# Kernel tuning notes

Hardware: AMD Instinct MI355X
Metric: run time of the kernel (lower is better)

Reference implementation:

```python
import jax, jax.numpy as jnp
import numpy as np
import math

N_HEADS = 16
D_MODEL = 1024
M = D_MODEL // N_HEADS  # per-head dim = 64

def _kaiming_uniform(key, shape):
    # torch kaiming_uniform_ with a=sqrt(5) on [h, fan_in, fan_out]-style 3D tensor:
    # fan_in = shape[1] (size of dim 1), gain = sqrt(2/(1+a^2)) = sqrt(1/3)
    fan_in = shape[1]
    gain = math.sqrt(2.0 / (1.0 + 5.0))
    bound = gain * math.sqrt(3.0 / fan_in)
    return jax.random.uniform(key, shape, dtype=jnp.float32, minval=-bound, maxval=bound)

def setup_inputs() -> dict:
    key = jax.random.key(0)
    kx, kq, kk, kv, ko = jax.random.split(key, 5)
    x = jax.random.normal(kx, (4, 2048, D_MODEL), dtype=jnp.float32)
    W_q = _kaiming_uniform(kq, (N_HEADS, D_MODEL, M))
    W_k = _kaiming_uniform(kk, (N_HEADS, D_MODEL, M))
    W_v = _kaiming_uniform(kv, (N_HEADS, D_MODEL, M))
    W_o = _kaiming_uniform(ko, (N_HEADS, M, D_MODEL))
    return {"x": x, "W_q": W_q, "W_k": W_k, "W_v": W_v, "W_o": W_o}

def reference(x, W_q, W_k, W_v, W_o):
    # x: [b, s, d]; W_q/W_k/W_v: [h, d, m]; W_o: [h, m, d]
    q = jnp.einsum('bsd,hdm->bhsm', x, W_q)
    k = jnp.einsum('bsd,hdm->bhsm', x, W_k)
    v = jnp.einsum('bsd,hdm->bhsm', x, W_v)
    scale = 1.0 / math.sqrt(q.shape[-1])
    scores = jnp.einsum('bhsm,bhtm->bhst', q, k) * scale  # [b,h,s,s]
    attn = jax.nn.softmax(scores, axis=-1)
    ctx = jnp.einsum('bhst,bhtm->bhsm', attn, v)
    out = jnp.einsum('bhsm,hmd->bsd', ctx, W_o)  # sum over heads
    return out
```

## Files before the change

kernel.cpp:

```cpp
#include <hip/hip_runtime.h>
#include <hip/hip_bf16.h>

typedef __attribute__((ext_vector_type(8))) short short8;
typedef __attribute__((ext_vector_type(8))) _Float16 half8;
typedef __attribute__((ext_vector_type(4))) float f32x4;
typedef __attribute__((ext_vector_type(16))) float f32x16;
typedef __attribute__((ext_vector_type(4))) unsigned int uint4v;

#define NB 4
#define NH 16
#define NS 2048
#define ND 1024
#define NM 64
#define R_TOT 8192
#define N_QKV 3072
#define QKV_ONE 8388608
#define SCALE_Q 0.18033688011112042f

static __device__ __forceinline__ unsigned short f2h(float f) {
    _Float16 h = (_Float16)f;
    return __builtin_bit_cast(unsigned short, h);
}
static __device__ __forceinline__ unsigned cvtpk_h(float lo, float hiv) {
    unsigned r;
    asm("v_cvt_pkrtz_f16_f32 %0, %1, %2" : "=v"(r) : "v"(lo), "v"(hiv));
    return r;
}
static __device__ __forceinline__ void gl_lds16(const unsigned short* g, unsigned short* l) {
    __builtin_amdgcn_global_load_lds((const __attribute__((address_space(1))) void*)g,
                                     (__attribute__((address_space(3))) void*)l, 16, 0, 0);
}
static __device__ __forceinline__ half8 rd_swz(const unsigned short* base, int row, int col) {
    int byte = (row << 7) + (col << 1);
    byte ^= (row & 7) << 4;
    return *(const half8*)((const char*)base + byte);
}

__global__ __launch_bounds__(256) void k_convert_x(const float* __restrict__ x,
                                                   unsigned short* __restrict__ xh) {
    int i = blockIdx.x * 256 + threadIdx.x;
    const float4* xp = (const float4*)x;
    float4 v = xp[i];
    ushort4 o;
    o.x = f2h(v.x); o.y = f2h(v.y); o.z = f2h(v.z); o.w = f2h(v.w);
    ((ushort4*)xh)[i] = o;
}

__global__ __launch_bounds__(256) void k_convert_wqkv(const float* __restrict__ Wq,
                                                      const float* __restrict__ Wk,
                                                      const float* __restrict__ Wv,
                                                      unsigned short* __restrict__ BT) {
    int i = blockIdx.x * 256 + threadIdx.x;
    int d = i & 1023;
    int n = i >> 10;
    int w = n >> 10;
    int h = (n >> 6) & 15;
    int m = n & 63;
    const float* W = (w == 0) ? Wq : ((w == 1) ? Wk : Wv);
    float v = W[((size_t)h * ND + d) * NM + m];
    if (w == 0) v *= SCALE_Q;
    BT[i] = f2h(v);
}

__global__ __launch_bounds__(256) void k_convert_wo(const float* __restrict__ Wo,
                                                    unsigned short* __restrict__ BTo) {
    int i = blockIdx.x * 256 + threadIdx.x;
    int n = i & 1023;
    int d = i >> 10;
    BTo[i] = f2h(Wo[(size_t)n * ND + d]);
}

__global__ __launch_bounds__(256) void k_gemm_qkv(const unsigned short* __restrict__ A,
                                                  const unsigned short* __restrict__ BT,
                                                  unsigned short* __restrict__ qkv) {
    __shared__ unsigned short As[128 * 64];
    __shared__ unsigned short Bs[128 * 64];
    int tid = threadIdx.x;
    int bx = blockIdx.x;
    int rt = bx & 63;
    int ct = bx >> 6;
    int r0 = rt * 128, c0 = ct * 128;
    int lane = tid & 63, wid = tid >> 6;
    int l15 = lane & 15, grp = lane >> 4;
    int wr = (wid >> 1) * 64, wc = (wid & 1) * 64;

    f32x4 acc[4][4] = {};

    for (int k0 = 0; k0 < 1024; k0 += 64) {
        #pragma unroll
        for (int i = 0; i < 4; ++i) {
            int seg = wid * 4 + i;
            int row = seg * 8 + (lane >> 3);
            int sch = (lane & 7) ^ (row & 7);
            gl_lds16(A + (size_t)(r0 + row) * 1024 + k0 + sch * 8, As + seg * 512 + lane * 8);
            gl_lds16(BT + (size_t)(c0 + row) * 1024 + k0 + sch * 8, Bs + seg * 512 + lane * 8);
        }
        __syncthreads();
        #pragma unroll
        for (int ks = 0; ks < 64; ks += 32) {
            half8 af[4], bf[4];
            #pragma unroll
            for (int i = 0; i < 4; ++i)
                af[i] = rd_swz(As, wr + i * 16 + l15, ks + grp * 8);
            #pragma unroll
            for (int j = 0; j < 4; ++j)
                bf[j] = rd_swz(Bs, wc + j * 16 + l15, ks + grp * 8);
            #pragma unroll
            for (int i = 0; i < 4; ++i)
                #pragma unroll
                for (int j = 0; j < 4; ++j)
                    acc[i][j] = __builtin_amdgcn_mfma_f32_16x16x32_f16(af[i], bf[j], acc[i][j], 0, 0, 0);
        }
        __syncthreads();
    }
    #pragma unroll
    for (int j = 0; j < 4; ++j) {
        int n_base = c0 + wc + j * 16;
        int w = n_base >> 10;
        int nh = n_base + l15;
        int h = (nh >> 6) & 15;
        int m = nh & 63;
        if (w == 2) {
            unsigned short* outp = qkv + 2 * (size_t)QKV_ONE;
            #pragma unroll
            for (int i = 0; i < 4; ++i) {
                int rb = r0 + wr + i * 16 + grp * 4;
                int bb = rb >> 11, s = rb & 2047;
                ushort4 pv;
                pv.x = f2h(acc[i][j][0]);
                pv.y = f2h(acc[i][j][1]);
                pv.z = f2h(acc[i][j][2]);
                pv.w = f2h(acc[i][j][3]);
                *(ushort4*)(outp + ((size_t)(bb * NH + h) * NM + m) * NS + s) = pv;
            }
        } else {
            unsigned short* outp = qkv + (size_t)w * QKV_ONE;
            #pragma unroll
            for (int i = 0; i < 4; ++i) {
                int rb = r0 + wr + i * 16 + grp * 4;
                #pragma unroll
                for (int reg = 0; reg < 4; ++reg) {
                    int r = rb + reg;
                    int bb = r >> 11, s = r & 2047;
                    outp[((size_t)(bb * NH + h) * NS + s) * NM + m] = f2h(acc[i][j][reg]);
                }
            }
        }
    }
}

__global__ __launch_bounds__(256) void k_attn(const unsigned short* __restrict__ qkv,
                                              unsigned short* __restrict__ ctx) {
    __shared__ unsigned short Ks[2][4096];
    __shared__ unsigned short Vs[2][4096];
    __shared__ float ls[4][32];

    int tid = threadIdx.x;
    int lane = tid & 63, wid = tid >> 6;
    int l31 = lane & 31, hi = lane >> 5;

    int bid = blockIdx.x;
    int xcd = bid & 7;
    int j = bid >> 3;
    int bh = xcd * 8 + (j >> 4);
    int qb = j & 15;
    int b = bh >> 4, h = bh & 15;

    size_t hb = (size_t)bh * NS * NM;
    const unsigned short* Qg = qkv + hb;
    const unsigned short* Kg = qkv + QKV_ONE + hb;
    const unsigned short* Vt = qkv + 2 * (size_t)QKV_ONE + hb;

    int q0 = qb * 128 + wid * 32;

    half8 qf[4];
    #pragma unroll
    for (int kk = 0; kk < 4; ++kk)
        qf[kk] = *(const half8*)(Qg + (size_t)(q0 + l31) * NM + kk * 16 + hi * 8);

    f32x16 accO0 = {}, accO1 = {};
    float lsum = 0.f;

    auto stage = [&](int bufi, int t0) {
        #pragma unroll
        for (int i = 0; i < 4; ++i) {
            int seg = wid * 4 + i;
            int off = (seg & 7) * 512 + lane * 8;
            int row = off >> 6;
            int sch = ((off >> 3) & 7) ^ (row & 7);
            if (seg < 8)
                gl_lds16(Kg + (size_t)(t0 + row) * NM + sch * 8, &Ks[bufi][off]);
            else
                gl_lds16(Vt + (size_t)row * NS + t0 + sch * 8, &Vs[bufi][off]);
        }
    };

    stage(0, 0);
    stage(1, 64);

    for (int t = 0; t < 32; ++t) {
        int buf = t & 1;
        if (t < 31) asm volatile("s_waitcnt vmcnt(4)" ::: "memory");
        else        asm volatile("s_waitcnt vmcnt(0)" ::: "memory");
        __builtin_amdgcn_s_barrier();
        __builtin_amdgcn_sched_barrier(0);
        const unsigned short* Kb = Ks[buf];
        const unsigned short* Vb = Vs[buf];

        f32x16 s0v = {}, s1v = {};
        __builtin_amdgcn_s_setprio(1);
        #pragma unroll
        for (int kk = 0; kk < 4; ++kk) {
            int col = kk * 16 + hi * 8;
            s0v = __builtin_amdgcn_mfma_f32_32x32x16_f16(rd_swz(Kb, l31, col), qf[kk], s0v, 0, 0, 0);
            s1v = __builtin_amdgcn_mfma_f32_32x32x16_f16(rd_swz(Kb, 32 + l31, col), qf[kk], s1v, 0, 0, 0);
        }
        __builtin_amdgcn_s_setprio(0);

        unsigned pk0[8], pk1[8];
        #pragma unroll
        for (int jj = 0; jj < 8; ++jj) {
            float a0 = __builtin_amdgcn_exp2f(s0v[2 * jj]);
            float b0 = __builtin_amdgcn_exp2f(s0v[2 * jj + 1]);
            float a1 = __builtin_amdgcn_exp2f(s1v[2 * jj]);
            float b1 = __builtin_amdgcn_exp2f(s1v[2 * jj + 1]);
            lsum += a0 + b0 + a1 + b1;
            pk0[jj] = cvtpk_h(a0, b0);
            pk1[jj] = cvtpk_h(a1, b1);
        }

        __builtin_amdgcn_s_setprio(1);
        #pragma unroll
        for (int kt = 0; kt < 4; ++kt) {
            unsigned w0, w1, w2, w3;
            if (kt < 2) {
                int base = (kt & 1) * 4;
                w0 = pk0[base + 0]; w1 = pk0[base + 1];
                w2 = pk0[base + 2]; w3 = pk0[base + 3];
            } else {
                int base = (kt & 1) * 4;
                w0 = pk1[base + 0]; w1 = pk1[base + 1];
                w2 = pk1[base + 2]; w3 = pk1[base + 3];
            }
            asm("v_permlane32_swap_b32 %0, %1" : "+v"(w0), "+v"(w2));
            asm("v_permlane32_swap_b32 %0, %1" : "+v"(w1), "+v"(w3));
            uint4v av;
            av[0] = w0; av[1] = w1; av[2] = w2; av[3] = w3;
            half8 af = __builtin_bit_cast(half8, av);
            int col = kt * 16 + hi * 8;
            accO0 = __builtin_amdgcn_mfma_f32_32x32x16_f16(af, rd_swz(Vb, l31, col), accO0, 0, 0, 0);
            accO1 = __builtin_amdgcn_mfma_f32_32x32x16_f16(af, rd_swz(Vb, 32 + l31, col), accO1, 0, 0, 0);
        }
        __builtin_amdgcn_s_setprio(0);

        __builtin_amdgcn_sched_barrier(0);
        __builtin_amdgcn_s_barrier();
        if (t < 30) stage(buf, (t + 2) * 64);
    }

    float lt = lsum + __shfl_xor(lsum, 32);
    ls[wid][l31] = lt;
    __syncthreads();

    #pragma unroll
    for (int reg = 0; reg < 16; ++reg) {
        int q = (reg & 3) + 8 * (reg >> 2) + 4 * hi;
        float linv = 1.0f / ls[wid][q];
        size_t ob = ((size_t)b * NS + (q0 + q)) * ND + h * 64 + l31;
        ctx[ob] = f2h(accO0[reg] * linv);
        ctx[ob + 32] = f2h(accO1[reg] * linv);
    }
}

__global__ __launch_bounds__(256) void k_gemm_out(const unsigned short* __restrict__ A,
                                                  const unsigned short* __restrict__ BT,
                                                  float* __restrict__ Cf) {
    __shared__ unsigned short As[128 * 64];
    __shared__ unsigned short Bs[128 * 64];
    int tid = threadIdx.x;
    int bx = blockIdx.x;
    int rt = bx & 63, ct = bx >> 6;
    int r0 = rt * 128, c0 = ct * 128;
    int lane = tid & 63, wid = tid >> 6;
    int l15 = lane & 15, grp = lane >> 4;
    int wr = (wid >> 1) * 64, wc = (wid & 1) * 64;
    f32x4 acc[4][4] = {};

    for (int k0 = 0; k0 < 1024; k0 += 64) {
        #pragma unroll
        for (int i = 0; i < 4; ++i) {
            int seg = wid * 4 + i;
            int row = seg * 8 + (lane >> 3);
            int sch = (lane & 7) ^ (row & 7);
            gl_lds16(A + (size_t)(r0 + row) * 1024 + k0 + sch * 8, As + seg * 512 + lane * 8);
            gl_lds16(BT + (size_t)(c0 + row) * 1024 + k0 + sch * 8, Bs + seg * 512 + lane * 8);
        }
        __syncthreads();
        #pragma unroll
        for (int ks = 0; ks < 64; ks += 32) {
            half8 af[4], bf[4];
            #pragma unroll
            for (int i = 0; i < 4; ++i)
                af[i] = rd_swz(As, wr + i * 16 + l15, ks + grp * 8);
            #pragma unroll
            for (int j = 0; j < 4; ++j)
                bf[j] = rd_swz(Bs, wc + j * 16 + l15, ks + grp * 8);
            #pragma unroll
            for (int i = 0; i < 4; ++i)
                #pragma unroll
                for (int j = 0; j < 4; ++j)
                    acc[i][j] = __builtin_amdgcn_mfma_f32_16x16x32_f16(af[i], bf[j], acc[i][j], 0, 0, 0);
        }
        __syncthreads();
    }
    #pragma unroll
    for (int i = 0; i < 4; ++i)
        #pragma unroll
        for (int j = 0; j < 4; ++j)
            #pragma unroll
            for (int reg = 0; reg < 4; ++reg) {
                int r = r0 + wr + i * 16 + grp * 4 + reg;
                int c = c0 + wc + j * 16 + l15;
                Cf[(size_t)r * 1024 + c] = acc[i][j][reg];
            }
}

extern "C" void kernel_launch(void* const* d_in, const int* in_sizes, int n_in,
                              void* d_out, int out_size, void* d_ws, size_t ws_size,
                              hipStream_t stream) {
    (void)in_sizes; (void)n_in; (void)out_size; (void)ws_size;
    const float* x  = (const float*)d_in[0];
    const float* Wq = (const float*)d_in[1];
    const float* Wk = (const float*)d_in[2];
    const float* Wv = (const float*)d_in[3];
    const float* Wo = (const float*)d_in[4];

    char* ws = (char*)d_ws;
    unsigned short* Xh   = (unsigned short*)ws;  ws += (size_t)R_TOT * 1024 * 2;
    unsigned short* BTq  = (unsigned short*)ws;  ws += (size_t)N_QKV * 1024 * 2;
    unsigned short* BTo  = (unsigned short*)ws;  ws += (size_t)1024 * 1024 * 2;
    unsigned short* QKV  = (unsigned short*)ws;  ws += (size_t)3 * QKV_ONE * 2;
    unsigned short* Ctx  = (unsigned short*)ws;  ws += (size_t)R_TOT * 1024 * 2;

    k_convert_x<<<dim3(R_TOT * 1024 / 4 / 256), dim3(256), 0, stream>>>(x, Xh);
    k_convert_wqkv<<<dim3(N_QKV * 1024 / 256), dim3(256), 0, stream>>>(Wq, Wk, Wv, BTq);
    k_convert_wo<<<dim3(1024 * 1024 / 256), dim3(256), 0, stream>>>(Wo, BTo);
    k_gemm_qkv<<<dim3(64 * 24), dim3(256), 0, stream>>>(Xh, BTq, QKV);
    k_attn<<<dim3(1024), dim3(256), 0, stream>>>(QKV, Ctx);
    k_gemm_out<<<dim3(64 * 8), dim3(256), 0, stream>>>(Ctx, BTo, (float*)d_out);
}
```

Baseline: 219.6 us.

## Double attention block size to 8 waves and compute row sums via MFMA

The attention kernel now runs 512-thread blocks covering 256 query rows, so each staged K/V tile is shared by twice as many waves and each thread issues half as many global-to-LDS loads. Stage addresses are precomputed outside the loop. The softmax row-sum moves from scalar adds plus a shared-memory reduction to an extra MFMA against a vector of ones, which removes the final barrier and LDS traffic. The cost is one more MFMA per PV step and fewer, larger blocks (512), which may reduce occupancy and latency hiding.

```diff
diff --git a/kernel.cpp b/kernel.cpp
--- a/kernel.cpp
+++ b/kernel.cpp
@@ -149,11 +149,10 @@
     }
 }
 
-__global__ __launch_bounds__(256) void k_attn(const unsigned short* __restrict__ qkv,
+__global__ __launch_bounds__(512) void k_attn(const unsigned short* __restrict__ qkv,
                                               unsigned short* __restrict__ ctx) {
     __shared__ unsigned short Ks[2][4096];
     __shared__ unsigned short Vs[2][4096];
-    __shared__ float ls[4][32];
 
     int tid = threadIdx.x;
     int lane = tid & 63, wid = tid >> 6;
@@ -162,8 +161,8 @@
     int bid = blockIdx.x;
     int xcd = bid & 7;
     int j = bid >> 3;
-    int bh = xcd * 8 + (j >> 4);
-    int qb = j & 15;
+    int bh = xcd * 8 + (j >> 3);
+    int qb = j & 7;
     int b = bh >> 4, h = bh & 15;
 
     size_t hb = (size_t)bh * NS * NM;
@@ -171,28 +170,41 @@
     const unsigned short* Kg = qkv + QKV_ONE + hb;
     const unsigned short* Vt = qkv + 2 * (size_t)QKV_ONE + hb;
 
-    int q0 = qb * 128 + wid * 32;
+    int q0 = qb * 256 + wid * 32;
 
     half8 qf[4];
     #pragma unroll
     for (int kk = 0; kk < 4; ++kk)
         qf[kk] = *(const half8*)(Qg + (size_t)(q0 + l31) * NM + kk * 16 + hi * 8);
 
-    f32x16 accO0 = {}, accO1 = {};
-    float lsum = 0.f;
-
+    half8 ones;
+    #pragma unroll
+    for (int e = 0; e < 8; ++e) ones[e] = (_Float16)1.0f;
+
+    f32x16 accO0 = {}, accO1 = {}, accS = {};
+
+    const unsigned short* gsrc0;
+    const unsigned short* gsrc1;
+    unsigned short* lbase0;
+    unsigned short* lbase1;
+    int step0, step1;
+    {
+        int seg = wid * 2;
+        int off = (seg & 7) * 512 + lane * 8;
+        int row = off >> 6;
+        int sch = ((off >> 3) & 7) ^ (row & 7);
+        if (seg < 8) { gsrc0 = Kg + row * NM + sch * 8; step0 = NM;  lbase0 = &Ks[0][off]; }
+        else         { gsrc0 = Vt + (size_t)row * NS + sch * 8; step0 = 1; lbase0 = &Vs[0][off]; }
+        seg = wid * 2 + 1;
+        off = (seg & 7) * 512 + lane * 8;
+        row = off >> 6;
+        sch = ((off >> 3) & 7) ^ (row & 7);
+        if (seg < 8) { gsrc1 = Kg + row * NM + sch * 8; step1 = NM;  lbase1 = &Ks[0][off]; }
+        else         { gsrc1 = Vt + (size_t)row * NS + sch * 8; step1 = 1; lbase1 = &Vs[0][off]; }
+    }
     auto stage = [&](int bufi, int t0) {
-        #pragma unroll
-        for (int i = 0; i < 4; ++i) {
-            int seg = wid * 4 + i;
-            int off = (seg & 7) * 512 + lane * 8;
-            int row = off >> 6;
-            int sch = ((off >> 3) & 7) ^ (row & 7);
-            if (seg < 8)
-                gl_lds16(Kg + (size_t)(t0 + row) * NM + sch * 8, &Ks[bufi][off]);
-            else
-                gl_lds16(Vt + (size_t)row * NS + t0 + sch * 8, &Vs[bufi][off]);
-        }
+        gl_lds16(gsrc0 + (size_t)t0 * step0, lbase0 + bufi * 4096);
+        gl_lds16(gsrc1 + (size_t)t0 * step1, lbase1 + bufi * 4096);
     };
 
     stage(0, 0);
@@ -200,7 +212,7 @@
 
     for (int t = 0; t < 32; ++t) {
         int buf = t & 1;
-        if (t < 31) asm volatile("s_waitcnt vmcnt(4)" ::: "memory");
+        if (t < 31) asm volatile("s_waitcnt vmcnt(2)" ::: "memory");
         else        asm volatile("s_waitcnt vmcnt(0)" ::: "memory");
         __builtin_amdgcn_s_barrier();
         __builtin_amdgcn_sched_barrier(0);
@@ -224,7 +236,6 @@
             float b0 = __builtin_amdgcn_exp2f(s0v[2 * jj + 1]);
             float a1 = __builtin_amdgcn_exp2f(s1v[2 * jj]);
             float b1 = __builtin_amdgcn_exp2f(s1v[2 * jj + 1]);
-            lsum += a0 + b0 + a1 + b1;
             pk0[jj] = cvtpk_h(a0, b0);
             pk1[jj] = cvtpk_h(a1, b1);
         }
@@ -250,6 +261,7 @@
             int col = kt * 16 + hi * 8;
             accO0 = __builtin_amdgcn_mfma_f32_32x32x16_f16(af, rd_swz(Vb, l31, col), accO0, 0, 0, 0);
             accO1 = __builtin_amdgcn_mfma_f32_32x32x16_f16(af, rd_swz(Vb, 32 + l31, col), accO1, 0, 0, 0);
+            accS  = __builtin_amdgcn_mfma_f32_32x32x16_f16(af, ones, accS, 0, 0, 0);
         }
         __builtin_amdgcn_s_setprio(0);
 
@@ -258,14 +270,10 @@
         if (t < 30) stage(buf, (t + 2) * 64);
     }
 
-    float lt = lsum + __shfl_xor(lsum, 32);
-    ls[wid][l31] = lt;
-    __syncthreads();
-
     #pragma unroll
     for (int reg = 0; reg < 16; ++reg) {
         int q = (reg & 3) + 8 * (reg >> 2) + 4 * hi;
-        float linv = 1.0f / ls[wid][q];
+        float linv = 1.0f / accS[reg];
         size_t ob = ((size_t)b * NS + (q0 + q)) * ND + h * 64 + l31;
         ctx[ob] = f2h(accO0[reg] * linv);
         ctx[ob + 32] = f2h(accO1[reg] * linv);
@@ -346,6 +354,6 @@
     k_convert_wqkv<<<dim3(N_QKV * 1024 / 256), dim3(256), 0, stream>>>(Wq, Wk, Wv, BTq);
     k_convert_wo<<<dim3(1024 * 1024 / 256), dim3(256), 0, stream>>>(Wo, BTo);
     k_gemm_qkv<<<dim3(64 * 24), dim3(256), 0, stream>>>(Xh, BTq, QKV);
-    k_attn<<<dim3(1024), dim3(256), 0, stream>>>(QKV, Ctx);
+    k_attn<<<dim3(512), dim3(512), 0, stream>>>(QKV, Ctx);
     k_gemm_out<<<dim3(64 * 8), dim3(256), 0, stream>>>(Ctx, BTo, (float*)d_out);
 }
```

Measured after the change: 198.6 us. 9.6% less time.
